# Kernel tuning notes

Measured on AMD Instinct MI355X. Metric: run time of the kernel, lower is better.

Reference implementation:

```python
import jax, jax.numpy as jnp
import numpy as np

N_NODES = 20000
C_IN = 128
C_OUT = 128
C_MID = 8            # max(C_IN // 16, 8) per TP.__init__
NEIGHBOR_CG = 8
INF = 1000000.0
EPS = 1e-5
# real spherical harmonics for l=1 are ordered (m=-1,0,1) ~ (y,z,x)
P_L1 = jnp.array([[0., 1., 0.], [0., 0., 1.], [1., 0., 0.]], dtype=jnp.float32)


def equivariant_layer_norm(x, ln_w, ln_b):
    # x: (N, 4, C); l=0 block x[:, :1], l=1 block x[:, 1:4]
    x0 = x[:, :1, :]
    x0 = x0 - jnp.mean(x0, axis=-1, keepdims=True)          # mean only for l=0
    n0 = jnp.mean(jnp.sum(x0 * x0, axis=1, keepdims=True), axis=-1, keepdims=True)
    y0 = x0 * jax.lax.rsqrt(n0 + EPS) * ln_w[0] + ln_b
    x1 = x[:, 1:4, :]
    n1 = jnp.mean(jnp.sum(x1 * x1, axis=1, keepdims=True), axis=-1, keepdims=True)
    y1 = x1 * jax.lax.rsqrt(n1 + EPS) * ln_w[1]
    return jnp.concatenate([y0, y1], axis=1)


def rotation_to_z(vec):
    # vec: (..., 3) -> R with R @ unit(vec) = z_hat (Rodrigues, safe at c ~ -1)
    n = jnp.linalg.norm(vec, axis=-1, keepdims=True)
    v = vec / (n + 1e-9)
    c = v[..., 2]
    kx, ky = v[..., 1], -v[..., 0]                 # k = v x z_hat = (v_y, -v_x, 0)
    zero = jnp.zeros_like(kx)
    K = jnp.stack([
        jnp.stack([zero, zero, ky], -1),
        jnp.stack([zero, zero, -kx], -1),
        jnp.stack([-ky, kx, zero], -1)], -2)
    safe = c > -0.999
    denom = jnp.where(safe, 1.0 + c, 1.0)
    I = jnp.eye(3, dtype=vec.dtype)
    R = I + K + jnp.matmul(K, K) / denom[..., None, None]
    flip = jnp.array([[1., 0., 0.], [0., -1., 0.], [0., 0., -1.]], dtype=vec.dtype)
    return jnp.where(safe[..., None, None], R, flip)


def escn_tensor_product(msg, vec, so2_w0, so2_wr, so2_wi):
    # msg: (N, H, 4, Cm), vec: (N, H, 3)
    R = rotation_to_z(vec)                                      # (N,H,3,3)
    D1 = jnp.einsum('ij,nhjk,lk->nhil', P_L1, R, P_L1)          # Wigner-D, l=1
    l1 = jnp.einsum('nhij,nhjc->nhic', D1, msg[..., 1:4, :])    # rotate to edge frame
    # m = 0 channel mix across degrees (l=0 coeff, l=1 m=0 coeff)
    m0_in = jnp.stack([msg[..., 0, :], l1[..., 1, :]], axis=-2)  # (N,H,2,Cm)
    m0 = (m0_in.reshape(m0_in.shape[:-2] + (2 * C_MID,)) @ so2_w0).reshape(m0_in.shape)
    # m = +/-1 SO(2) convolution
    x_m1, x_p1 = l1[..., 0, :], l1[..., 2, :]
    y_p1 = x_p1 @ so2_wr - x_m1 @ so2_wi
    y_m1 = x_m1 @ so2_wr + x_p1 @ so2_wi
    out_l1 = jnp.stack([y_m1, m0[..., 1, :], y_p1], axis=-2)     # (N,H,3,Cm)
    out_l1 = jnp.einsum('nhji,nhjc->nhic', D1, out_l1)           # rotate back (D1^T)
    return jnp.concatenate([m0[..., :1, :], out_l1], axis=-2)    # (N,H,4,Cm)


def setup_inputs() -> dict:
    key = jax.random.key(0)
    ks = jax.random.split(key, 10)
    s_feats = jax.random.normal(ks[0], (N_NODES, 4, C_IN), jnp.float32)
    s_points = jax.random.normal(ks[1], (N_NODES, 3), jnp.float32) * 5.0
    neighbor_indices = jax.random.randint(ks[2], (N_NODES, 9), 0, N_NODES + 1)
    ln_w = 1.0 + 0.02 * jax.random.normal(ks[3], (2, C_IN), jnp.float32)
    ln_b = 0.02 * jax.random.normal(ks[4], (C_IN,), jnp.float32)
    w_in = jax.random.normal(ks[5], (2 * C_IN, C_MID), jnp.float32) / np.sqrt(2 * C_IN)
    w_out = jax.random.normal(ks[6], (C_MID, C_OUT), jnp.float32) / np.sqrt(C_MID)
    so2_w0 = jax.random.normal(ks[7], (2 * C_MID, 2 * C_MID), jnp.float32) / np.sqrt(2 * C_MID)
    so2_wr = jax.random.normal(ks[8], (C_MID, C_MID), jnp.float32) / np.sqrt(C_MID)
    so2_wi = jax.random.normal(ks[9], (C_MID, C_MID), jnp.float32) / np.sqrt(C_MID)
    return dict(s_feats=s_feats, s_points=s_points, neighbor_indices=neighbor_indices,
                ln_w=ln_w, ln_b=ln_b, w_in=w_in, w_out=w_out,
                so2_w0=so2_w0, so2_wr=so2_wr, so2_wi=so2_wi)


def reference(s_feats, s_points, neighbor_indices, ln_w, ln_b, w_in, w_out, so2_w0, so2_wr, so2_wi):
    N = s_feats.shape[0]
    x = equivariant_layer_norm(s_feats, ln_w, ln_b)                  # (N,4,C)
    sp_pad = jnp.concatenate([s_points, jnp.full((1, 3), INF, s_points.dtype)], 0)
    x_pad = jnp.concatenate([x, jnp.zeros_like(x[:1])], 0)
    idx = neighbor_indices[:, 1:]                                     # drop self
    mask = (idx < N).astype(x.dtype)                                  # (N,Hfull)
    npts = (sp_pad[idx] * mask[..., None])[:, :NEIGHBOR_CG]           # (N,H,3)
    nfts = (x_pad[idx] * mask[..., None, None])[:, :NEIGHBOR_CG]      # (N,H,4,C)
    vec = npts - s_points[:, None, :]                                 # (N,H,3)
    sfe = jnp.broadcast_to(x[:, None], nfts.shape)                    # (N,H,4,C)
    msg = jnp.concatenate([nfts, sfe], axis=-1) @ w_in                # (N,H,4,Cm)
    msg = escn_tensor_product(msg, vec, so2_w0, so2_wr, so2_wi)       # (N,H,4,Cm)
    out = msg.sum(axis=1) @ w_out                                     # (N,4,C_out)
    return out
```

## Files before the change

### kernel.cpp

```cpp
#include <hip/hip_runtime.h>
#include <math.h>

#define SWZ8(x)  __int_as_float(__builtin_amdgcn_ds_swizzle(__float_as_int(x), 0x201F))
#define SWZ16(x) __int_as_float(__builtin_amdgcn_ds_swizzle(__float_as_int(x), 0x401F))
#define SX32(x)  __shfl_xor((x), 32)

__global__ __launch_bounds__(256, 4) void k1_ln_proj(
    const float* __restrict__ s_feats,
    const float* __restrict__ ln_w,
    const float* __restrict__ ln_b,
    const float* __restrict__ w_in,
    float* __restrict__ ys,
    int N)
{
    const int lane = threadIdx.x & 63;
    const int kq = lane & 7;
    const int cg = lane >> 3;
    const int n = blockIdx.x * 4 + (threadIdx.x >> 6);

    float wa0[16], wa1[16], wb0[16], wb1[16];
    float B1 = 0.f, C1 = 0.f, B2 = 0.f, C2 = 0.f;
    #pragma unroll
    for (int t = 0; t < 16; t++) {
        int c = cg * 16 + t;
        float w1 = w_in[c * 8 + kq];
        float w2 = w_in[(128 + c) * 8 + kq];
        float l0 = ln_w[c], l1 = ln_w[128 + c], lb = ln_b[c];
        wa0[t] = w1 * l0; wa1[t] = w1 * l1;
        wb0[t] = w2 * l0; wb1[t] = w2 * l1;
        B1 += w1 * l0; C1 += lb * w1;
        B2 += w2 * l0; C2 += lb * w2;
    }
    B1 += SWZ8(B1);  C1 += SWZ8(C1);  B2 += SWZ8(B2);  C2 += SWZ8(C2);
    B1 += SWZ16(B1); C1 += SWZ16(C1); B2 += SWZ16(B2); C2 += SWZ16(C2);
    B1 += SX32(B1);  C1 += SX32(C1);  B2 += SX32(B2);  C2 += SX32(C2);

    if (n >= N) return;

    const float* sp = s_feats + (size_t)n * 512 + cg * 16;
    float accY[4] = {0.f, 0.f, 0.f, 0.f};
    float accS[4] = {0.f, 0.f, 0.f, 0.f};
    float ssum = 0.f, sq0 = 0.f, sq1 = 0.f;
    #pragma unroll
    for (int m = 0; m < 4; m++) {
        #pragma unroll
        for (int i = 0; i < 4; i++) {
            float4 v = *(const float4*)(sp + m * 128 + i * 4);
            float e0 = v.x, e1 = v.y, e2 = v.z, e3 = v.w;
            if (m == 0) {
                accY[0] += e0 * wa0[i*4+0] + e1 * wa0[i*4+1] + e2 * wa0[i*4+2] + e3 * wa0[i*4+3];
                accS[0] += e0 * wb0[i*4+0] + e1 * wb0[i*4+1] + e2 * wb0[i*4+2] + e3 * wb0[i*4+3];
                ssum += e0 + e1 + e2 + e3;
                sq0  += e0 * e0 + e1 * e1 + e2 * e2 + e3 * e3;
            } else {
                accY[m] += e0 * wa1[i*4+0] + e1 * wa1[i*4+1] + e2 * wa1[i*4+2] + e3 * wa1[i*4+3];
                accS[m] += e0 * wb1[i*4+0] + e1 * wb1[i*4+1] + e2 * wb1[i*4+2] + e3 * wb1[i*4+3];
                sq1  += e0 * e0 + e1 * e1 + e2 * e2 + e3 * e3;
            }
        }
    }
    #define RED_ALL(FN) \
        accY[0] += FN(accY[0]); accY[1] += FN(accY[1]); accY[2] += FN(accY[2]); accY[3] += FN(accY[3]); \
        accS[0] += FN(accS[0]); accS[1] += FN(accS[1]); accS[2] += FN(accS[2]); accS[3] += FN(accS[3]); \
        ssum += FN(ssum); sq0 += FN(sq0); sq1 += FN(sq1);
    RED_ALL(SWZ8)
    RED_ALL(SWZ16)
    RED_ALL(SX32)
    #undef RED_ALL

    float mean = ssum * (1.0f / 128.0f);
    float r0 = rsqrtf((sq0 - ssum * mean) * (1.0f / 128.0f) + 1e-5f);
    float r1 = rsqrtf(sq1 * (1.0f / 128.0f) + 1e-5f);

    float aA = (cg & 2) ? ((cg & 1) ? accY[3] : accY[2]) : ((cg & 1) ? accY[1] : accY[0]);
    float aB = (cg & 2) ? ((cg & 1) ? accS[3] : accS[2]) : ((cg & 1) ? accS[1] : accS[0]);
    float av = (cg & 4) ? aB : aA;
    float Bv = (cg & 4) ? B2 : B1;
    float Cv = (cg & 4) ? C2 : C1;
    bool isM0 = (cg & 3) == 0;
    float outv = isM0 ? (r0 * (av - mean * Bv) + Cv) : (r1 * av);
    ys[(size_t)n * 64 + kq * 4 + (cg & 3) + ((cg & 4) << 3)] = outv;
}

#define TROW 36

__global__ __launch_bounds__(256, 4) void k2_edges(
    const float* __restrict__ ys,
    const float* __restrict__ s_points,
    const int*   __restrict__ nbr,
    const float* __restrict__ w0,
    const float* __restrict__ wr,
    const float* __restrict__ wi,
    const float* __restrict__ w_out,
    float* __restrict__ out,
    int N)
{
    __shared__ float tbuf[4][8 * TROW];
    __shared__ float abuf[4][32];

    const int lane = threadIdx.x & 63;
    const int h = lane >> 3, k = lane & 7;
    const int wv = threadIdx.x >> 6;
    const int n = blockIdx.x * 4 + wv;

    float c00[8], c08[8], c10[8], c18[8], cwr[8], cwi[8];
    #pragma unroll
    for (int j = 0; j < 8; j++) {
        c00[j] = w0[j * 16 + k];
        c08[j] = w0[(8 + j) * 16 + k];
        c10[j] = w0[j * 16 + 8 + k];
        c18[j] = w0[(8 + j) * 16 + 8 + k];
        cwr[j] = wr[j * 8 + k];
        cwi[j] = wi[j * 8 + k];
    }
    float wc0[8], wc1[8];
    #pragma unroll
    for (int kk = 0; kk < 8; kk++) {
        float2 w2v = *(const float2*)&w_out[kk * 128 + lane * 2];
        wc0[kk] = w2v.x; wc1[kk] = w2v.y;
    }

    if (n >= N) return;

    int idx = nbr[n * 9 + 1 + h];
    bool mk = idx < N;
    float px = s_points[n * 3], py = s_points[n * 3 + 1], pz = s_points[n * 3 + 2];
    float nx = mk ? s_points[idx * 3]     : 0.f;
    float ny = mk ? s_points[idx * 3 + 1] : 0.f;
    float nz = mk ? s_points[idx * 3 + 2] : 0.f;
    float vx = nx - px, vy = ny - py, vz = nz - pz;
    float nn = sqrtf(vx * vx + vy * vy + vz * vz);
    float inv = 1.0f / (nn + 1e-9f);
    float ux = vx * inv, uy = vy * inv, uz = vz * inv;
    float cz = uz;
    float kx = uy, ky = -ux;
    bool safe = cz > -0.999f;
    float id = safe ? 1.0f / (1.0f + cz) : 1.0f;
    float D1[3][3];
    {
        float R00, R01, R02, R10, R11, R12, R20, R21, R22;
        if (safe) {
            R00 = 1.0f - ky * ky * id; R01 = kx * ky * id;        R02 = ky;
            R10 = kx * ky * id;        R11 = 1.0f - kx * kx * id; R12 = -kx;
            R20 = -ky;                 R21 = kx;                  R22 = 1.0f - (kx * kx + ky * ky) * id;
        } else {
            R00 = 1.0f; R01 = 0.0f; R02 = 0.0f;
            R10 = 0.0f; R11 = -1.0f; R12 = 0.0f;
            R20 = 0.0f; R21 = 0.0f; R22 = -1.0f;
        }
        D1[0][0] = R11; D1[0][1] = R12; D1[0][2] = R10;
        D1[1][0] = R21; D1[1][1] = R22; D1[1][2] = R20;
        D1[2][0] = R01; D1[2][1] = R02; D1[2][2] = R00;
    }

    float4 yv = mk ? *(const float4*)(ys + (size_t)idx * 64 + k * 4)
                   : float4{0.f, 0.f, 0.f, 0.f};
    float4 sv = *(const float4*)(ys + (size_t)n * 64 + 32 + k * 4);
    float msg0 = yv.x + sv.x;
    float msg1 = yv.y + sv.y;
    float msg2 = yv.z + sv.z;
    float msg3 = yv.w + sv.w;

    float l1_0 = D1[0][0] * msg1 + D1[0][1] * msg2 + D1[0][2] * msg3;
    float l1_1 = D1[1][0] * msg1 + D1[1][1] * msg2 + D1[1][2] * msg3;
    float l1_2 = D1[2][0] * msg1 + D1[2][1] * msg2 + D1[2][2] * msg3;

    *(float4*)&tbuf[wv][h * TROW + k * 4] = float4{msg0, l1_0, l1_1, l1_2};

    float m00 = 0.f, m01 = 0.f, ypl = 0.f, yml = 0.f;
    #pragma unroll
    for (int j = 0; j < 8; j++) {
        float4 t = *(const float4*)&tbuf[wv][h * TROW + j * 4];
        m00 += t.x * c00[j] + t.z * c08[j];
        m01 += t.x * c10[j] + t.z * c18[j];
        ypl += t.w * cwr[j] - t.y * cwi[j];
        yml += t.y * cwr[j] + t.w * cwi[j];
    }

    float f0 = m00;
    float f1 = D1[0][0] * yml + D1[1][0] * m01 + D1[2][0] * ypl;
    float f2 = D1[0][1] * yml + D1[1][1] * m01 + D1[2][1] * ypl;
    float f3 = D1[0][2] * yml + D1[1][2] * m01 + D1[2][2] * ypl;

    f0 += SWZ8(f0);  f1 += SWZ8(f1);  f2 += SWZ8(f2);  f3 += SWZ8(f3);
    f0 += SWZ16(f0); f1 += SWZ16(f1); f2 += SWZ16(f2); f3 += SWZ16(f3);
    f0 += SX32(f0);  f1 += SX32(f1);  f2 += SX32(f2);  f3 += SX32(f3);

    if (lane < 8)
        *(float4*)&abuf[wv][lane * 4] = float4{f0, f1, f2, f3};

    float o0[4] = {0.f, 0.f, 0.f, 0.f}, o1[4] = {0.f, 0.f, 0.f, 0.f};
    #pragma unroll
    for (int kk = 0; kk < 8; kk++) {
        float4 a = *(const float4*)&abuf[wv][kk * 4];
        o0[0] += a.x * wc0[kk]; o1[0] += a.x * wc1[kk];
        o0[1] += a.y * wc0[kk]; o1[1] += a.y * wc1[kk];
        o0[2] += a.z * wc0[kk]; o1[2] += a.z * wc1[kk];
        o0[3] += a.w * wc0[kk]; o1[3] += a.w * wc1[kk];
    }
    float* op = out + (size_t)n * 512;
    #pragma unroll
    for (int m = 0; m < 4; m++)
        *(float2*)(op + m * 128 + lane * 2) = float2{o0[m], o1[m]};
}

extern "C" void kernel_launch(void* const* d_in, const int* in_sizes, int n_in,
                              void* d_out, int out_size, void* d_ws, size_t ws_size,
                              hipStream_t stream) {
    const float* s_feats  = (const float*)d_in[0];
    const float* s_points = (const float*)d_in[1];
    const int*   nbr      = (const int*)d_in[2];
    const float* ln_w     = (const float*)d_in[3];
    const float* ln_b     = (const float*)d_in[4];
    const float* w_in     = (const float*)d_in[5];
    const float* w_out    = (const float*)d_in[6];
    const float* so2_w0   = (const float*)d_in[7];
    const float* so2_wr   = (const float*)d_in[8];
    const float* so2_wi   = (const float*)d_in[9];
    float* out = (float*)d_out;

    int N = in_sizes[0] / 512;
    float* ys = (float*)d_ws;

    int nb = (N + 3) / 4;
    k1_ln_proj<<<nb, 256, 0, stream>>>(s_feats, ln_w, ln_b, w_in, ys, N);
    k2_edges<<<nb, 256, 0, stream>>>(ys, s_points, nbr, so2_w0, so2_wr, so2_wi,
                                     w_out, out, N);
}
```

Measured before the change: 54.71 us.

## Process two nodes per wave in edge kernel and coalesce projection stores

The edge kernel now handles two nodes per wavefront, issuing all gathers for both nodes up front and spreading the per-thread weight register loads over twice the work. Launching half as many blocks is meant to cut that weight-loading overhead and raise memory-level parallelism. The projection kernel uses a lane shuffle so each wave writes its 64 outputs contiguously, and it reads s_feats with nontemporal loads. The cost is more registers and LDS per block, which may lower occupancy.

New measurement: 68.10 us. +24.5%, slower.

```diff
diff --git a/kernel.cpp b/kernel.cpp
--- a/kernel.cpp
+++ b/kernel.cpp
@@ -1,5 +1,8 @@
 #include <hip/hip_runtime.h>
 #include <math.h>
+
+typedef float fx4 __attribute__((ext_vector_type(4)));
+typedef float fx2 __attribute__((ext_vector_type(2)));
 
 #define SWZ8(x)  __int_as_float(__builtin_amdgcn_ds_swizzle(__float_as_int(x), 0x201F))
 #define SWZ16(x) __int_as_float(__builtin_amdgcn_ds_swizzle(__float_as_int(x), 0x401F))
@@ -45,7 +48,7 @@
     for (int m = 0; m < 4; m++) {
         #pragma unroll
         for (int i = 0; i < 4; i++) {
-            float4 v = *(const float4*)(sp + m * 128 + i * 4);
+            fx4 v = __builtin_nontemporal_load((const fx4*)(sp + m * 128 + i * 4));
             float e0 = v.x, e1 = v.y, e2 = v.z, e3 = v.w;
             if (m == 0) {
                 accY[0] += e0 * wa0[i*4+0] + e1 * wa0[i*4+1] + e2 * wa0[i*4+2] + e3 * wa0[i*4+3];
@@ -79,10 +82,13 @@
     float Cv = (cg & 4) ? C2 : C1;
     bool isM0 = (cg & 3) == 0;
     float outv = isM0 ? (r0 * (av - mean * Bv) + Cv) : (r1 * av);
-    ys[(size_t)n * 64 + kq * 4 + (cg & 3) + ((cg & 4) << 3)] = outv;
+
+    int src = ((lane >> 2) & 7) + ((lane & 3) << 3) + (lane & 32);
+    float myv = __shfl(outv, src);
+    ys[(size_t)n * 64 + lane] = myv;
 }
 
-#define TROW 36
+#define TROW 40
 
 __global__ __launch_bounds__(256, 4) void k2_edges(
     const float* __restrict__ ys,
@@ -95,13 +101,14 @@
     float* __restrict__ out,
     int N)
 {
-    __shared__ float tbuf[4][8 * TROW];
-    __shared__ float abuf[4][32];
-
-    const int lane = threadIdx.x & 63;
+    __shared__ float tbuf[8][8 * TROW];
+    __shared__ float abuf[8][32];
+
+    const int tid = threadIdx.x;
+    const int lane = tid & 63;
     const int h = lane >> 3, k = lane & 7;
-    const int wv = threadIdx.x >> 6;
-    const int n = blockIdx.x * 4 + wv;
+    const int wv = tid >> 6;
+    const int base = (blockIdx.x * 4 + wv) * 2;
 
     float c00[8], c08[8], c10[8], c18[8], cwr[8], cwi[8];
     #pragma unroll
@@ -116,92 +123,105 @@
     float wc0[8], wc1[8];
     #pragma unroll
     for (int kk = 0; kk < 8; kk++) {
-        float2 w2v = *(const float2*)&w_out[kk * 128 + lane * 2];
+        fx2 w2v = *(const fx2*)&w_out[kk * 128 + lane * 2];
         wc0[kk] = w2v.x; wc1[kk] = w2v.y;
     }
 
-    if (n >= N) return;
-
-    int idx = nbr[n * 9 + 1 + h];
-    bool mk = idx < N;
-    float px = s_points[n * 3], py = s_points[n * 3 + 1], pz = s_points[n * 3 + 2];
-    float nx = mk ? s_points[idx * 3]     : 0.f;
-    float ny = mk ? s_points[idx * 3 + 1] : 0.f;
-    float nz = mk ? s_points[idx * 3 + 2] : 0.f;
-    float vx = nx - px, vy = ny - py, vz = nz - pz;
-    float nn = sqrtf(vx * vx + vy * vy + vz * vz);
-    float inv = 1.0f / (nn + 1e-9f);
-    float ux = vx * inv, uy = vy * inv, uz = vz * inv;
-    float cz = uz;
-    float kx = uy, ky = -ux;
-    bool safe = cz > -0.999f;
-    float id = safe ? 1.0f / (1.0f + cz) : 1.0f;
-    float D1[3][3];
-    {
-        float R00, R01, R02, R10, R11, R12, R20, R21, R22;
-        if (safe) {
-            R00 = 1.0f - ky * ky * id; R01 = kx * ky * id;        R02 = ky;
-            R10 = kx * ky * id;        R11 = 1.0f - kx * kx * id; R12 = -kx;
-            R20 = -ky;                 R21 = kx;                  R22 = 1.0f - (kx * kx + ky * ky) * id;
-        } else {
-            R00 = 1.0f; R01 = 0.0f; R02 = 0.0f;
-            R10 = 0.0f; R11 = -1.0f; R12 = 0.0f;
-            R20 = 0.0f; R21 = 0.0f; R22 = -1.0f;
-        }
-        D1[0][0] = R11; D1[0][1] = R12; D1[0][2] = R10;
-        D1[1][0] = R21; D1[1][1] = R22; D1[1][2] = R20;
-        D1[2][0] = R01; D1[2][1] = R02; D1[2][2] = R00;
-    }
-
-    float4 yv = mk ? *(const float4*)(ys + (size_t)idx * 64 + k * 4)
-                   : float4{0.f, 0.f, 0.f, 0.f};
-    float4 sv = *(const float4*)(ys + (size_t)n * 64 + 32 + k * 4);
-    float msg0 = yv.x + sv.x;
-    float msg1 = yv.y + sv.y;
-    float msg2 = yv.z + sv.z;
-    float msg3 = yv.w + sv.w;
-
-    float l1_0 = D1[0][0] * msg1 + D1[0][1] * msg2 + D1[0][2] * msg3;
-    float l1_1 = D1[1][0] * msg1 + D1[1][1] * msg2 + D1[1][2] * msg3;
-    float l1_2 = D1[2][0] * msg1 + D1[2][1] * msg2 + D1[2][2] * msg3;
-
-    *(float4*)&tbuf[wv][h * TROW + k * 4] = float4{msg0, l1_0, l1_1, l1_2};
-
-    float m00 = 0.f, m01 = 0.f, ypl = 0.f, yml = 0.f;
-    #pragma unroll
-    for (int j = 0; j < 8; j++) {
-        float4 t = *(const float4*)&tbuf[wv][h * TROW + j * 4];
-        m00 += t.x * c00[j] + t.z * c08[j];
-        m01 += t.x * c10[j] + t.z * c18[j];
-        ypl += t.w * cwr[j] - t.y * cwi[j];
-        yml += t.y * cwr[j] + t.w * cwi[j];
-    }
-
-    float f0 = m00;
-    float f1 = D1[0][0] * yml + D1[1][0] * m01 + D1[2][0] * ypl;
-    float f2 = D1[0][1] * yml + D1[1][1] * m01 + D1[2][1] * ypl;
-    float f3 = D1[0][2] * yml + D1[1][2] * m01 + D1[2][2] * ypl;
-
-    f0 += SWZ8(f0);  f1 += SWZ8(f1);  f2 += SWZ8(f2);  f3 += SWZ8(f3);
-    f0 += SWZ16(f0); f1 += SWZ16(f1); f2 += SWZ16(f2); f3 += SWZ16(f3);
-    f0 += SX32(f0);  f1 += SX32(f1);  f2 += SX32(f2);  f3 += SX32(f3);
-
-    if (lane < 8)
-        *(float4*)&abuf[wv][lane * 4] = float4{f0, f1, f2, f3};
-
-    float o0[4] = {0.f, 0.f, 0.f, 0.f}, o1[4] = {0.f, 0.f, 0.f, 0.f};
-    #pragma unroll
-    for (int kk = 0; kk < 8; kk++) {
-        float4 a = *(const float4*)&abuf[wv][kk * 4];
-        o0[0] += a.x * wc0[kk]; o1[0] += a.x * wc1[kk];
-        o0[1] += a.y * wc0[kk]; o1[1] += a.y * wc1[kk];
-        o0[2] += a.z * wc0[kk]; o1[2] += a.z * wc1[kk];
-        o0[3] += a.w * wc0[kk]; o1[3] += a.w * wc1[kk];
-    }
-    float* op = out + (size_t)n * 512;
-    #pragma unroll
-    for (int m = 0; m < 4; m++)
-        *(float2*)(op + m * 128 + lane * 2) = float2{o0[m], o1[m]};
+    if (base >= N) return;
+    const int n1 = base + 1;
+    const bool v1 = n1 < N;
+
+    int idx0 = nbr[base * 9 + 1 + h];
+    int idx1 = v1 ? nbr[n1 * 9 + 1 + h] : 0x7fffffff;
+    bool mk0 = idx0 < N, mk1 = idx1 < N;
+
+    float px0 = s_points[base * 3], py0 = s_points[base * 3 + 1], pz0 = s_points[base * 3 + 2];
+    float px1 = v1 ? s_points[n1 * 3]     : 0.f;
+    float py1 = v1 ? s_points[n1 * 3 + 1] : 0.f;
+    float pz1 = v1 ? s_points[n1 * 3 + 2] : 0.f;
+    float nx0 = mk0 ? s_points[idx0 * 3]     : 0.f;
+    float ny0 = mk0 ? s_points[idx0 * 3 + 1] : 0.f;
+    float nz0 = mk0 ? s_points[idx0 * 3 + 2] : 0.f;
+    float nx1 = mk1 ? s_points[idx1 * 3]     : 0.f;
+    float ny1 = mk1 ? s_points[idx1 * 3 + 1] : 0.f;
+    float nz1 = mk1 ? s_points[idx1 * 3 + 2] : 0.f;
+    fx4 yv0 = mk0 ? *(const fx4*)(ys + (size_t)idx0 * 64 + k * 4) : (fx4){0.f,0.f,0.f,0.f};
+    fx4 yv1 = mk1 ? *(const fx4*)(ys + (size_t)idx1 * 64 + k * 4) : (fx4){0.f,0.f,0.f,0.f};
+    fx4 sv0 = *(const fx4*)(ys + (size_t)base * 64 + 32 + k * 4);
+    fx4 sv1 = v1 ? *(const fx4*)(ys + (size_t)n1 * 64 + 32 + k * 4) : (fx4){0.f,0.f,0.f,0.f};
+
+    auto node_compute = [&](int slot, int nn, float PX, float PY, float PZ,
+                            float NX, float NY, float NZ, fx4 YV, fx4 SV) {
+        float vx = NX - PX, vy = NY - PY, vz = NZ - PZ;
+        float nrm = sqrtf(vx * vx + vy * vy + vz * vz);
+        float inv = 1.0f / (nrm + 1e-9f);
+        float ux = vx * inv, uy = vy * inv, uz = vz * inv;
+        float cz = uz;
+        float kx = uy, ky = -ux;
+        bool safe = cz > -0.999f;
+        float idd = safe ? 1.0f / (1.0f + cz) : 1.0f;
+        float D00, D01, D02, D10, D11, D12, D20, D21, D22;
+        {
+            float R00, R01, R02, R10, R11, R12, R20, R21, R22;
+            if (safe) {
+                R00 = 1.0f - ky * ky * idd; R01 = kx * ky * idd;        R02 = ky;
+                R10 = kx * ky * idd;        R11 = 1.0f - kx * kx * idd; R12 = -kx;
+                R20 = -ky;                  R21 = kx;                   R22 = 1.0f - (kx * kx + ky * ky) * idd;
+            } else {
+                R00 = 1.0f; R01 = 0.0f; R02 = 0.0f;
+                R10 = 0.0f; R11 = -1.0f; R12 = 0.0f;
+                R20 = 0.0f; R21 = 0.0f; R22 = -1.0f;
+            }
+            D00 = R11; D01 = R12; D02 = R10;
+            D10 = R21; D11 = R22; D12 = R20;
+            D20 = R01; D21 = R02; D22 = R00;
+        }
+        float msg0 = YV.x + SV.x, msg1 = YV.y + SV.y, msg2 = YV.z + SV.z, msg3 = YV.w + SV.w;
+        float l1_0 = D00 * msg1 + D01 * msg2 + D02 * msg3;
+        float l1_1 = D10 * msg1 + D11 * msg2 + D12 * msg3;
+        float l1_2 = D20 * msg1 + D21 * msg2 + D22 * msg3;
+
+        *(fx4*)&tbuf[slot][h * TROW + k * 4] = (fx4){msg0, l1_0, l1_1, l1_2};
+
+        float m00 = 0.f, m01 = 0.f, ypl = 0.f, yml = 0.f;
+        #pragma unroll
+        for (int j = 0; j < 8; j++) {
+            fx4 t = *(const fx4*)&tbuf[slot][h * TROW + j * 4];
+            m00 += t.x * c00[j] + t.z * c08[j];
+            m01 += t.x * c10[j] + t.z * c18[j];
+            ypl += t.w * cwr[j] - t.y * cwi[j];
+            yml += t.y * cwr[j] + t.w * cwi[j];
+        }
+        float f0 = m00;
+        float f1 = D00 * yml + D10 * m01 + D20 * ypl;
+        float f2 = D01 * yml + D11 * m01 + D21 * ypl;
+        float f3 = D02 * yml + D12 * m01 + D22 * ypl;
+
+        f0 += SWZ8(f0);  f1 += SWZ8(f1);  f2 += SWZ8(f2);  f3 += SWZ8(f3);
+        f0 += SWZ16(f0); f1 += SWZ16(f1); f2 += SWZ16(f2); f3 += SWZ16(f3);
+        f0 += SX32(f0);  f1 += SX32(f1);  f2 += SX32(f2);  f3 += SX32(f3);
+
+        if (h == 0)
+            *(fx4*)&abuf[slot][k * 4] = (fx4){f0, f1, f2, f3};
+
+        float o0[4] = {0.f, 0.f, 0.f, 0.f}, o1[4] = {0.f, 0.f, 0.f, 0.f};
+        #pragma unroll
+        for (int kk = 0; kk < 8; kk++) {
+            fx4 a = *(const fx4*)&abuf[slot][kk * 4];
+            o0[0] += a.x * wc0[kk]; o1[0] += a.x * wc1[kk];
+            o0[1] += a.y * wc0[kk]; o1[1] += a.y * wc1[kk];
+            o0[2] += a.z * wc0[kk]; o1[2] += a.z * wc1[kk];
+            o0[3] += a.w * wc0[kk]; o1[3] += a.w * wc1[kk];
+        }
+        float* op = out + (size_t)nn * 512;
+        #pragma unroll
+        for (int m = 0; m < 4; m++)
+            *(fx2*)(op + m * 128 + lane * 2) = (fx2){o0[m], o1[m]};
+    };
+
+    node_compute(wv * 2 + 0, base, px0, py0, pz0, nx0, ny0, nz0, yv0, sv0);
+    if (v1)
+        node_compute(wv * 2 + 1, n1, px1, py1, pz1, nx1, ny1, nz1, yv1, sv1);
 }
 
 extern "C" void kernel_launch(void* const* d_in, const int* in_sizes, int n_in,
@@ -222,8 +242,9 @@
     int N = in_sizes[0] / 512;
     float* ys = (float*)d_ws;
 
-    int nb = (N + 3) / 4;
-    k1_ln_proj<<<nb, 256, 0, stream>>>(s_feats, ln_w, ln_b, w_in, ys, N);
-    k2_edges<<<nb, 256, 0, stream>>>(ys, s_points, nbr, so2_w0, so2_wr, so2_wi,
-                                     w_out, out, N);
+    int nb1 = (N + 3) / 4;
+    int nb2 = (N + 7) / 8;
+    k1_ln_proj<<<nb1, 256, 0, stream>>>(s_feats, ln_w, ln_b, w_in, ys, N);
+    k2_edges<<<nb2, 256, 0, stream>>>(ys, s_points, nbr, so2_w0, so2_wr, so2_wi,
+                                      w_out, out, N);
 }
```
